# Kernel tuning notes

Hardware: AMD Instinct MI355X
Metric: run time of the kernel (lower is better)

Reference implementation:

```python
import jax, jax.numpy as jnp
import numpy as np

HEADS = 8
D_MODEL = 512

def setup_inputs() -> dict:
    key = jax.random.key(0)
    ks = jax.random.split(key, 7)
    t, w, h, b = 8, 14, 14, 8
    seq = t * w * h + 1  # 1569, includes CLS token
    q = jax.random.normal(ks[0], (seq, b, D_MODEL), jnp.float32)
    k = jax.random.normal(ks[1], (seq, b, D_MODEL), jnp.float32)
    value = jax.random.normal(ks[2], (seq, b, D_MODEL), jnp.float32)
    in_proj_weight = jax.random.normal(ks[3], (3 * D_MODEL, D_MODEL), jnp.float32) * (D_MODEL ** -0.5)
    in_proj_bias = jax.random.normal(ks[4], (3 * D_MODEL,), jnp.float32) * 0.02
    out_w = jax.random.normal(ks[5], (D_MODEL, D_MODEL), jnp.float32) * (D_MODEL ** -0.5)
    out_b = jax.random.normal(ks[6], (D_MODEL,), jnp.float32) * 0.02
    return {"q": q, "k": k, "value": value,
            "in_proj_weight": in_proj_weight, "in_proj_bias": in_proj_bias,
            "out_w": out_w, "out_b": out_b, "t": t, "w": w, "h": h}

def _sdpa(q, k, v):
    # scaled dot-product attention over batched 3D tensors [B, L, dh]
    temp = q.shape[-1] ** 0.5
    scores = jnp.einsum('bqd,bkd->bqk', q, k) / temp
    a = jax.nn.softmax(scores, axis=-1)  # softmax over dim=2 == last dim
    return jnp.einsum('bqk,bkd->bqd', a, v), a

def reference(q, k, value, in_proj_weight, in_proj_bias, out_w, out_b, t, w, h):
    seq, b, c = q.shape
    H, dh, wh = HEADS, c // HEADS, w * h
    q_cls = q[:1]          # [1, b, c] passed through untouched
    x = q[1:]              # [t*wh, b, c]
    qkv = x @ in_proj_weight.T + in_proj_bias  # fused QKV proj
    qq, kk, vv = qkv[..., :c], qkv[..., c:2 * c], qkv[..., 2 * c:]
    to5 = lambda z: z.reshape(t, wh, b, H, dh)
    # spatial stage: batch = (H, b, t), attend over wh
    q_s = to5(qq).transpose(3, 2, 0, 1, 4).reshape(H * b * t, wh, dh)
    k_s = to5(kk).transpose(3, 2, 0, 1, 4).reshape(H * b * t, wh, dh)
    v_s = to5(vv).transpose(3, 2, 0, 1, 4).reshape(H * b * t, wh, dh)
    out_s, attn = _sdpa(q_s, k_s, v_s)
    # temporal stage: batch = (H, b, wh), attend over t; V comes from spatial output
    v_t = out_s.reshape(H, b, t, wh, dh).transpose(0, 1, 3, 2, 4).reshape(H * b * wh, t, dh)
    q_t = to5(qq).transpose(3, 2, 1, 0, 4).reshape(H * b * wh, t, dh)
    k_t = to5(kk).transpose(3, 2, 1, 0, 4).reshape(H * b * wh, t, dh)
    out_t, _ = _sdpa(q_t, k_t, v_t)
    # back to [t*wh, b, c]
    out = out_t.reshape(H, b, wh, t, dh).transpose(3, 2, 1, 0, 4).reshape(t * wh, b, c)
    out = out @ out_w.T + out_b
    return jnp.concatenate([q_cls, out], axis=0), attn
```

## Files before the change

### kernel.cpp

```cpp
#include <hip/hip_runtime.h>
#include <cstdint>
#include <cstddef>

typedef __bf16 bf16;
typedef __bf16 bf16x8 __attribute__((ext_vector_type(8)));
typedef __bf16 bf16x4 __attribute__((ext_vector_type(4)));
typedef float  f32x4  __attribute__((ext_vector_type(4)));

#define MFMA16(a, b, c) __builtin_amdgcn_mfma_f32_16x16x32_bf16(a, b, c, 0, 0, 0)

__device__ __forceinline__ void gl2lds16(const bf16* g, bf16* l) {
  __builtin_amdgcn_global_load_lds(
      (const __attribute__((address_space(1))) void*)g,
      (__attribute__((address_space(3))) void*)l, 16, 0, 0);
}

__device__ __forceinline__ void cvt4(const float* __restrict__ s, bf16* __restrict__ d) {
  f32x4 v = *(const f32x4*)s;
  bf16x4 o;
  o[0] = (bf16)v[0]; o[1] = (bf16)v[1]; o[2] = (bf16)v[2]; o[3] = (bf16)v[3];
  *(bf16x4*)d = o;
}

__global__ __launch_bounds__(256) void prep_kernel(
    const float* __restrict__ q, const float* __restrict__ win,
    const float* __restrict__ wout, float* __restrict__ out0,
    bf16* __restrict__ xb, bf16* __restrict__ wqb, bf16* __restrict__ wob) {
  long u = (long)blockIdx.x * 256 + threadIdx.x;
  const long NX4 = 1605632, NWQ4 = 196608, NWO4 = 65536, NQC4 = 1024;
  if (u < NX4) { cvt4(q + 4096 + u * 4, xb + u * 4); return; }
  u -= NX4;
  if (u < NWQ4) { cvt4(win + u * 4, wqb + u * 4); return; }
  u -= NWQ4;
  if (u < NWO4) { cvt4(wout + u * 4, wob + u * 4); return; }
  u -= NWO4;
  if (u < NQC4) { *(f32x4*)(out0 + u * 4) = *(const f32x4*)(q + u * 4); }
}

template <bool OUTF32>
__global__ __launch_bounds__(256) void gemm_bt(
    const bf16* __restrict__ A, const bf16* __restrict__ Bm,
    const float* __restrict__ bias, bf16* __restrict__ Cb,
    float* __restrict__ Cf, int N, int K, long coff) {
  __shared__ bf16 As[128 * 32];
  __shared__ bf16 Bs[128 * 32];
  const int tid = threadIdx.x;
  const int wid = tid >> 6, lane = tid & 63;
  const int lr = lane & 15, lg = lane >> 4;

  const int nwg = gridDim.x * gridDim.y;
  const int orig = blockIdx.y * gridDim.x + blockIdx.x;
  const int cpx = nwg >> 3;
  const int swz = (orig & 7) * cpx + (orig >> 3);
  const int m0 = (swz / gridDim.x) * 128;
  const int n0 = (swz % gridDim.x) * 128;

  const int wr = wid >> 1, wc = wid & 1;
  const int srow = lane >> 2;
  const int scol = (lane & 3) * 8;

  f32x4 acc[4][4] = {};

  for (int kt = 0; kt < K; kt += 32) {
    __syncthreads();
#pragma unroll
    for (int j = 0; j < 2; ++j) {
      int r0 = wid * 32 + j * 16;
      gl2lds16(A + (size_t)(m0 + r0 + srow) * K + kt + scol, As + r0 * 32);
      gl2lds16(Bm + (size_t)(n0 + r0 + srow) * K + kt + scol, Bs + r0 * 32);
    }
    __syncthreads();

    bf16x8 af[4], bfr[4];
#pragma unroll
    for (int m = 0; m < 4; ++m)
      af[m] = *(const bf16x8*)(As + (wr * 64 + m * 16 + lr) * 32 + lg * 8);
#pragma unroll
    for (int n = 0; n < 4; ++n)
      bfr[n] = *(const bf16x8*)(Bs + (wc * 64 + n * 16 + lr) * 32 + lg * 8);
#pragma unroll
    for (int m = 0; m < 4; ++m)
#pragma unroll
      for (int n = 0; n < 4; ++n)
        acc[m][n] = MFMA16(af[m], bfr[n], acc[m][n]);
  }

#pragma unroll
  for (int m = 0; m < 4; ++m) {
    int row = m0 + wr * 64 + m * 16 + lg * 4;
#pragma unroll
    for (int n = 0; n < 4; ++n) {
      int col = n0 + wc * 64 + n * 16 + lr;
      float bv = bias[col];
#pragma unroll
      for (int i = 0; i < 4; ++i) {
        float v = acc[m][n][i] + bv;
        if (OUTF32)
          __builtin_nontemporal_store(v, Cf + coff + (size_t)(row + i) * N + col);
        else
          Cb[(size_t)(row + i) * N + col] = (bf16)v;
      }
    }
  }
}

__global__ __launch_bounds__(1024) void spatial_attn(
    const bf16* __restrict__ qkv, float* __restrict__ attn_out,
    bf16* __restrict__ outs) {
  __shared__ bf16 Kl[224][72];
  __shared__ bf16 Vt[64][232];
  __shared__ bf16 StgB[13 * 3136];

  const int tid = threadIdx.x;
  const int wid = tid >> 6, lane = tid & 63;
  const int lr = lane & 15, lg = lane >> 4;
  const int batch = blockIdx.x;
  const int ti = batch & 7;
  const int bb = (batch >> 3) & 7;
  const int h = batch >> 6;

  {
    const int p = (tid >> 3);
    const int c = (tid & 7) * 8;
    bf16 zz = (bf16)0.f;
#pragma unroll
    for (int r0 = 0; r0 < 256; r0 += 128) {
      int pp = r0 + p;
      bf16x8 kv = {zz, zz, zz, zz, zz, zz, zz, zz};
      if (pp < 196) {
        size_t ro = ((size_t)(ti * 196 + pp) * 8 + bb) * 1536 + h * 64 + c;
        kv = *(const bf16x8*)(qkv + ro + 512);
      }
      if (pp < 224) *(bf16x8*)&Kl[pp][c] = kv;
    }
  }
  {
    const int c = (wid & 7) * 8;
    const int rbase = (wid >> 3) * 64 + lane;
    bf16 zz = (bf16)0.f;
#pragma unroll
    for (int r0 = 0; r0 < 256; r0 += 128) {
      int pp = r0 + rbase;
      bf16x8 vv = {zz, zz, zz, zz, zz, zz, zz, zz};
      if (pp < 196) {
        size_t ro = ((size_t)(ti * 196 + pp) * 8 + bb) * 1536 + h * 64 + c;
        vv = *(const bf16x8*)(qkv + ro + 1024);
      }
      if (pp < 224) {
#pragma unroll
        for (int j = 0; j < 8; ++j) Vt[c + j][pp] = vv[j];
      }
    }
  }
  __syncthreads();

  const int qt = wid;
  if (qt < 13) {
    const int q = qt * 16 + lr;
    bf16x8 aq[2];
    {
      int row = q > 195 ? 195 : q;
      size_t ro = ((size_t)(ti * 196 + row) * 8 + bb) * 1536 + h * 64;
#pragma unroll
      for (int kk = 0; kk < 2; ++kk)
        aq[kk] = *(const bf16x8*)(qkv + ro + kk * 32 + lg * 8);
    }

    f32x4 s[14] = {};
#pragma unroll
    for (int nn = 0; nn < 14; ++nn) {
      bf16x8 bk0 = *(const bf16x8*)&Kl[nn * 16 + lr][lg * 8];
      bf16x8 bk1 = *(const bf16x8*)&Kl[nn * 16 + lr][32 + lg * 8];
      s[nn] = MFMA16(bk0, aq[0], s[nn]);
      s[nn] = MFMA16(bk1, aq[1], s[nn]);
    }

#pragma unroll
    for (int nn = 0; nn < 14; ++nn) {
      bool pad = (nn * 16 + lg * 4 >= 196);
#pragma unroll
      for (int i = 0; i < 4; ++i)
        s[nn][i] = pad ? -1e30f : s[nn][i] * 0.125f;
    }

    float v = -1e30f;
#pragma unroll
    for (int nn = 0; nn < 14; ++nn)
#pragma unroll
      for (int i = 0; i < 4; ++i) v = fmaxf(v, s[nn][i]);
    v = fmaxf(v, __shfl_xor(v, 16));
    v = fmaxf(v, __shfl_xor(v, 32));
    float sum = 0.f;
#pragma unroll
    for (int nn = 0; nn < 14; ++nn)
#pragma unroll
      for (int i = 0; i < 4; ++i) {
        float e = __expf(s[nn][i] - v);
        s[nn][i] = e;
        sum += e;
      }
    sum += __shfl_xor(sum, 16);
    sum += __shfl_xor(sum, 32);
    const float rinv = 1.f / sum;

    bf16* const tile = StgB + qt * 3136;
    const int low = lr + 32 * (lg & 1);
    const int high = low + 16;
    const bool hiN = (lg >> 1) != 0;
    f32x4 o[4] = {};
#pragma unroll
    for (int kb = 0; kb < 7; ++kb) {
      uint32_t px[2], py[2];
#pragma unroll
      for (int t = 0; t < 2; ++t) {
        const int nn = 2 * kb + t;
        f32x4 sv;
#pragma unroll
        for (int i = 0; i < 4; ++i) sv[i] = s[nn][i] * rinv;
        union { bf16x4 h; uint2 u; } pk;
        pk.h[0] = (bf16)sv[0]; pk.h[1] = (bf16)sv[1];
        pk.h[2] = (bf16)sv[2]; pk.h[3] = (bf16)sv[3];
        int kbase = nn * 16 + lg * 4;
        if (kbase < 196)
          *(uint2*)((char*)tile + lr * 392 + kbase * 2) = pk.u;
        px[t] = pk.u.x; py[t] = pk.u.y;
      }
      uint32_t a0x = __shfl((int)px[0], low);
      uint32_t a0y = __shfl((int)py[0], low);
      uint32_t a1x = __shfl((int)px[1], low);
      uint32_t a1y = __shfl((int)py[1], low);
      uint32_t b0x = __shfl((int)px[0], high);
      uint32_t b0y = __shfl((int)py[0], high);
      uint32_t b1x = __shfl((int)px[1], high);
      uint32_t b1y = __shfl((int)py[1], high);
      union { uint32_t u[4]; bf16x8 h; } pa;
      pa.u[0] = hiN ? a1x : a0x;
      pa.u[1] = hiN ? a1y : a0y;
      pa.u[2] = hiN ? b1x : b0x;
      pa.u[3] = hiN ? b1y : b0y;
#pragma unroll
      for (int nd = 0; nd < 4; ++nd) {
        bf16x8 vb = *(const bf16x8*)&Vt[nd * 16 + lr][kb * 32 + lg * 8];
        o[nd] = MFMA16(pa.h, vb, o[nd]);
      }
    }

#pragma unroll
    for (int i = 0; i < 4; ++i) {
      int p = qt * 16 + lg * 4 + i;
      if (p < 196) {
#pragma unroll
        for (int nd = 0; nd < 4; ++nd) {
          int d = nd * 16 + lr;
          outs[(((size_t)((h * 8 + bb) * 196 + p)) * 8 + ti) * 64 + d] =
              (bf16)o[nd][i];
        }
      }
    }

    {
      const int vbytes = (qt == 12) ? 3136 : 12544;
      char* dst = (char*)(attn_out + (size_t)batch * 38416 + qt * 3136);
      const char* src = (const char*)tile;
#pragma unroll
      for (int j = 0; j < 13; ++j) {
        int x = j * 1024 + lane * 16;
        if (x < vbytes) {
          uint2 u = *(const uint2*)(src + (x >> 1));
          union { uint32_t b; float f; } c0, c1, c2, c3;
          c0.b = (u.x & 0xffffu) << 16; c1.b = u.x & 0xffff0000u;
          c2.b = (u.y & 0xffffu) << 16; c3.b = u.y & 0xffff0000u;
          f32x4 ov; ov[0] = c0.f; ov[1] = c1.f; ov[2] = c2.f; ov[3] = c3.f;
          *(f32x4*)(dst + x) = ov;
        }
      }
    }
  }
}

__global__ __launch_bounds__(256) void temporal_attn(
    const bf16* __restrict__ qkv, const bf16* __restrict__ outs,
    bf16* __restrict__ outt) {
  __shared__ bf16 Ql[4][8][72];
  __shared__ bf16 Kc[4][8][72];
  __shared__ bf16 Vl[4][8][64];
  __shared__ float Ps[4][8][8];

  const int tid = threadIdx.x, wid = tid >> 6, lane = tid & 63;
  const int batch = blockIdx.x * 4 + wid;
  const int p = batch % 196;
  const int hb = batch / 196;
  const int bb = hb & 7, h = hb >> 3;

  const int ri = lane >> 3;
  const int c8 = lane & 7;
  {
    size_t ro = ((size_t)(ri * 196 + p) * 8 + bb) * 1536 + h * 64 + c8 * 8;
    *(bf16x8*)&Ql[wid][ri][c8 * 8] = *(const bf16x8*)(qkv + ro);
    *(bf16x8*)&Kc[wid][ri][c8 * 8] = *(const bf16x8*)(qkv + ro + 512);
    *(bf16x8*)&Vl[wid][ri][c8 * 8] =
        *(const bf16x8*)(outs + ((size_t)batch * 8 + ri) * 64 + c8 * 8);
  }
  __syncthreads();

  float s = 0.f;
#pragma unroll
  for (int d = 0; d < 64; d += 8) {
    bf16x8 qv = *(const bf16x8*)&Ql[wid][ri][d];
    bf16x8 kv = *(const bf16x8*)&Kc[wid][c8][d];
#pragma unroll
    for (int e = 0; e < 8; ++e) s += (float)qv[e] * (float)kv[e];
  }
  s *= 0.125f;
  float mxv = s;
#pragma unroll
  for (int d2 = 1; d2 < 8; d2 <<= 1) mxv = fmaxf(mxv, __shfl_xor(mxv, d2));
  float e = __expf(s - mxv);
  float sum = e;
#pragma unroll
  for (int d2 = 1; d2 < 8; d2 <<= 1) sum += __shfl_xor(sum, d2);
  Ps[wid][ri][c8] = e / sum;
  __syncthreads();

  const int d = lane;
#pragma unroll
  for (int ii = 0; ii < 8; ++ii) {
    float o = 0.f;
#pragma unroll
    for (int j = 0; j < 8; ++j) o += Ps[wid][ii][j] * (float)Vl[wid][j][d];
    outt[((size_t)(ii * 196 + p) * 8 + bb) * 512 + h * 64 + d] = (bf16)o;
  }
}

extern "C" void kernel_launch(void* const* d_in, const int* in_sizes, int n_in,
                              void* d_out, int out_size, void* d_ws,
                              size_t ws_size, hipStream_t stream) {
  (void)in_sizes; (void)n_in; (void)out_size; (void)ws_size;
  const float* q    = (const float*)d_in[0];
  const float* win  = (const float*)d_in[3];
  const float* bin  = (const float*)d_in[4];
  const float* wout = (const float*)d_in[5];
  const float* bout = (const float*)d_in[6];
  float* out0 = (float*)d_out;
  float* attn = out0 + 6426624L;

  bf16* qkv  = (bf16*)d_ws;
  bf16* outs = qkv + 19267584L;
  bf16* outt = outs + 6422528L;
  bf16* wob  = outt + 6422528L;

  bf16* xb  = (bf16*)attn;
  bf16* wqb = xb + 6422528L;

  prep_kernel<<<7300, 256, 0, stream>>>(q, win, wout, out0, xb, wqb, wob);
  gemm_bt<false><<<dim3(12, 98), 256, 0, stream>>>(xb, wqb, bin, qkv, nullptr,
                                                   1536, 512, 0);
  spatial_attn<<<512, 1024, 0, stream>>>(qkv, attn, outs);
  temporal_attn<<<3136, 256, 0, stream>>>(qkv, outs, outt);
  gemm_bt<true><<<dim3(4, 98), 256, 0, stream>>>(outt, wob, bout, nullptr,
                                                 out0, 512, 512, 4096);
}
```

Baseline: 102.9 us.

## Load K tile via direct global-to-LDS with XOR swizzle and hoist Q loads

Spatial attention now brings the K tile into shared memory with global_load_lds DMA into an unpadded, XOR-swizzled layout instead of register round-trips into a padded array. The read side applies the same swizzle so MFMA operand reads stay free of bank conflicts. Q fragment loads move ahead of the barrier so they overlap the K/V staging. Padded rows are clamped to row 195 rather than zeroed, relying on the existing score masking. s_setprio hints are added around the MFMA loops.

```diff
diff --git a/kernel.cpp b/kernel.cpp
--- a/kernel.cpp
+++ b/kernel.cpp
@@ -107,7 +107,7 @@
 __global__ __launch_bounds__(1024) void spatial_attn(
     const bf16* __restrict__ qkv, float* __restrict__ attn_out,
     bf16* __restrict__ outs) {
-  __shared__ bf16 Kl[224][72];
+  __shared__ bf16 Kl[224 * 64];
   __shared__ bf16 Vt[64][232];
   __shared__ bf16 StgB[13 * 3136];
 
@@ -120,60 +120,64 @@
   const int h = batch >> 6;
 
   {
-    const int p = (tid >> 3);
-    const int c = (tid & 7) * 8;
-    bf16 zz = (bf16)0.f;
-#pragma unroll
-    for (int r0 = 0; r0 < 256; r0 += 128) {
-      int pp = r0 + p;
-      bf16x8 kv = {zz, zz, zz, zz, zz, zz, zz, zz};
-      if (pp < 196) {
-        size_t ro = ((size_t)(ti * 196 + pp) * 8 + bb) * 1536 + h * 64 + c;
-        kv = *(const bf16x8*)(qkv + ro + 512);
-      }
-      if (pp < 224) *(bf16x8*)&Kl[pp][c] = kv;
+    const int slot = lane & 7, r8 = lane >> 3;
+    const int chunk = slot ^ r8;
+#pragma unroll
+    for (int t = 0; t < 2; ++t) {
+      int j = wid + t * 16;
+      if (j < 28) {
+        int row = j * 8 + r8;
+        int grow = row > 195 ? 195 : row;
+        const bf16* src = qkv +
+            ((size_t)(ti * 196 + grow) * 8 + bb) * 1536 + h * 64 + 512 +
+            chunk * 8;
+        gl2lds16(src, Kl + j * 512);
+      }
     }
   }
   {
     const int c = (wid & 7) * 8;
     const int rbase = (wid >> 3) * 64 + lane;
-    bf16 zz = (bf16)0.f;
 #pragma unroll
     for (int r0 = 0; r0 < 256; r0 += 128) {
       int pp = r0 + rbase;
-      bf16x8 vv = {zz, zz, zz, zz, zz, zz, zz, zz};
-      if (pp < 196) {
-        size_t ro = ((size_t)(ti * 196 + pp) * 8 + bb) * 1536 + h * 64 + c;
-        vv = *(const bf16x8*)(qkv + ro + 1024);
-      }
       if (pp < 224) {
+        int gp = pp > 195 ? 195 : pp;
+        bf16x8 vv = *(const bf16x8*)(
+            qkv + ((size_t)(ti * 196 + gp) * 8 + bb) * 1536 + h * 64 + 1024 + c);
 #pragma unroll
         for (int j = 0; j < 8; ++j) Vt[c + j][pp] = vv[j];
       }
     }
   }
+
+  const int qt = wid;
+  bf16x8 aq[2];
+  if (qt < 13) {
+    int row = qt * 16 + lr;
+    if (row > 195) row = 195;
+    size_t ro = ((size_t)(ti * 196 + row) * 8 + bb) * 1536 + h * 64;
+#pragma unroll
+    for (int kk = 0; kk < 2; ++kk)
+      aq[kk] = *(const bf16x8*)(qkv + ro + kk * 32 + lg * 8);
+  }
   __syncthreads();
 
-  const int qt = wid;
   if (qt < 13) {
     const int q = qt * 16 + lr;
-    bf16x8 aq[2];
-    {
-      int row = q > 195 ? 195 : q;
-      size_t ro = ((size_t)(ti * 196 + row) * 8 + bb) * 1536 + h * 64;
-#pragma unroll
-      for (int kk = 0; kk < 2; ++kk)
-        aq[kk] = *(const bf16x8*)(qkv + ro + kk * 32 + lg * 8);
-    }
+    const int x7 = lr & 7;
 
     f32x4 s[14] = {};
+    __builtin_amdgcn_s_setprio(1);
 #pragma unroll
     for (int nn = 0; nn < 14; ++nn) {
-      bf16x8 bk0 = *(const bf16x8*)&Kl[nn * 16 + lr][lg * 8];
-      bf16x8 bk1 = *(const bf16x8*)&Kl[nn * 16 + lr][32 + lg * 8];
+      const int krow = nn * 16 + lr;
+      bf16x8 bk0 = *(const bf16x8*)&Kl[krow * 64 + ((lg ^ x7) * 8)];
+      bf16x8 bk1 = *(const bf16x8*)&Kl[krow * 64 + (((4 + lg) ^ x7) * 8)];
       s[nn] = MFMA16(bk0, aq[0], s[nn]);
       s[nn] = MFMA16(bk1, aq[1], s[nn]);
     }
+    __builtin_amdgcn_s_setprio(0);
 
 #pragma unroll
     for (int nn = 0; nn < 14; ++nn) {
@@ -238,11 +242,13 @@
       pa.u[1] = hiN ? a1y : a0y;
       pa.u[2] = hiN ? b1x : b0x;
       pa.u[3] = hiN ? b1y : b0y;
+      __builtin_amdgcn_s_setprio(1);
 #pragma unroll
       for (int nd = 0; nd < 4; ++nd) {
         bf16x8 vb = *(const bf16x8*)&Vt[nd * 16 + lr][kb * 32 + lg * 8];
         o[nd] = MFMA16(pa.h, vb, o[nd]);
       }
+      __builtin_amdgcn_s_setprio(0);
     }
 
 #pragma unroll
```

Measured after the change: 102.4 us. Within noise of the previous version (-0.4%).
